# Performance work log

Measured on AMD Instinct MI355X. Metric: run time of the kernel, lower is better.

## Reference

```python
import jax, jax.numpy as jnp
import numpy as np

EMBED_DIM = 1024
NUM_HEADS = 16
HEAD_DIM = EMBED_DIM // NUM_HEADS
B, SQ, SKV = 2, 2048, 2048


def setup_inputs() -> dict:
    key = jax.random.key(0)
    ks = jax.random.split(key, 12)
    s = 1.0 / np.sqrt(EMBED_DIM)
    inp = {
        "query": jax.random.normal(ks[0], (B, SQ, EMBED_DIM), jnp.float32),
        "key": jax.random.normal(ks[1], (B, SKV, EMBED_DIM), jnp.float32),
        "value": jax.random.normal(ks[2], (B, SKV, EMBED_DIM), jnp.float32),
        "Wq": jax.random.normal(ks[3], (EMBED_DIM, EMBED_DIM), jnp.float32) * s,
        "bq": jnp.zeros((EMBED_DIM,), jnp.float32),
        "Wk": jax.random.normal(ks[4], (EMBED_DIM, EMBED_DIM), jnp.float32) * s,
        "bk": jnp.zeros((EMBED_DIM,), jnp.float32),
        "Wv": jax.random.normal(ks[5], (EMBED_DIM, EMBED_DIM), jnp.float32) * s,
        "bv": jnp.zeros((EMBED_DIM,), jnp.float32),
        "Wo": jax.random.normal(ks[6], (EMBED_DIM, EMBED_DIM), jnp.float32) * s,
        "bo": jnp.zeros((EMBED_DIM,), jnp.float32),
        "ln_gamma": jnp.ones((EMBED_DIM,), jnp.float32),
        "ln_beta": jnp.zeros((EMBED_DIM,), jnp.float32),
    }
    return inp


def reference(query, key, value, Wq, bq, Wk, bk, Wv, bv, Wo, bo, ln_gamma, ln_beta):
    b, sq, d = query.shape
    skv = key.shape[1]
    residual = query
    # projections -> [b, h, s, hd]
    Q = (query @ Wq + bq).reshape(b, sq, NUM_HEADS, HEAD_DIM).transpose(0, 2, 1, 3)
    K = (key @ Wk + bk).reshape(b, skv, NUM_HEADS, HEAD_DIM).transpose(0, 2, 1, 3)
    V = (value @ Wv + bv).reshape(b, skv, NUM_HEADS, HEAD_DIM).transpose(0, 2, 1, 3)
    scores = jnp.einsum("bhqd,bhkd->bhqk", Q, K) / jnp.sqrt(jnp.float32(HEAD_DIM)).astype(Q.dtype)
    attn = jax.nn.softmax(scores, axis=-1)  # dropout identity in eval
    attended = jnp.einsum("bhqk,bhkd->bhqd", attn, V)
    attended = attended.transpose(0, 2, 1, 3).reshape(b, sq, d)
    out = attended @ Wo + bo
    x = out + residual
    mu = jnp.mean(x, axis=-1, keepdims=True)
    var = jnp.var(x, axis=-1, keepdims=True)
    return (x - mu) / jnp.sqrt(var + 1e-5) * ln_gamma + ln_beta
```

## Files before the change

kernel.cpp:

```cpp
#include <hip/hip_runtime.h>

#define EMBED 1024
#define NHEAD 16
#define HDIM  64
#define BATCH 2
#define SEQ   2048
#define ROWS  (BATCH*SEQ)

typedef __bf16 bf16x8 __attribute__((ext_vector_type(8)));
typedef float  f32x4  __attribute__((ext_vector_type(4)));
typedef float  f32x16 __attribute__((ext_vector_type(16)));
typedef unsigned short u16x8 __attribute__((ext_vector_type(8)));
typedef unsigned short u16x4 __attribute__((ext_vector_type(4)));

__device__ __forceinline__ unsigned short f2bf(float f) {
    unsigned int u = __float_as_uint(f);
    u += 0x7FFFu + ((u >> 16) & 1u);
    return (unsigned short)(u >> 16);
}
__device__ __forceinline__ f32x4 zero4() { f32x4 z = {0.f, 0.f, 0.f, 0.f}; return z; }

__device__ __forceinline__ unsigned int cvtpk_bf16(float lo, float hi) {
    unsigned int r;
    asm("v_cvt_pk_bf16_f32 %0, %1, %2" : "=v"(r) : "v"(lo), "v"(hi));
    return r;
}
__device__ __forceinline__ void pl32swap(unsigned int &a, unsigned int &b) {
    asm("v_permlane32_swap_b32 %0, %1" : "+v"(a), "+v"(b));
}
__device__ __forceinline__ float exp2_hw(float x) {
    float r;
    asm("v_exp_f32 %0, %1" : "=v"(r) : "v"(x));
    return r;
}

__device__ __forceinline__ void gl_lds16(const unsigned short* g, unsigned short* l) {
    __builtin_amdgcn_global_load_lds(
        (const __attribute__((address_space(1))) void*)g,
        (__attribute__((address_space(3))) void*)l, 16, 0, 0);
}

__global__ __launch_bounds__(256) void cvt3_kernel(const float* __restrict__ q,
                                                   const float* __restrict__ k,
                                                   const float* __restrict__ v,
                                                   unsigned short* __restrict__ qo,
                                                   unsigned short* __restrict__ ko,
                                                   unsigned short* __restrict__ vo) {
    const float* in; unsigned short* out;
    if (blockIdx.y == 0)      { in = q; out = qo; }
    else if (blockIdx.y == 1) { in = k; out = ko; }
    else                      { in = v; out = vo; }
    int i = (blockIdx.x * 256 + threadIdx.x) * 4;
    float4 vv = *(const float4*)(in + i);
    u16x4 o = {f2bf(vv.x), f2bf(vv.y), f2bf(vv.z), f2bf(vv.w)};
    *(u16x4*)(out + i) = o;
}

__global__ __launch_bounds__(256) void transpose4_kernel(const float* __restrict__ w0,
                                                         const float* __restrict__ w1,
                                                         const float* __restrict__ w2,
                                                         const float* __restrict__ w3,
                                                         unsigned short* __restrict__ o0,
                                                         unsigned short* __restrict__ o1,
                                                         unsigned short* __restrict__ o2,
                                                         unsigned short* __restrict__ o3) {
    const float* in; unsigned short* out;
    if (blockIdx.z == 0)      { in = w0; out = o0; }
    else if (blockIdx.z == 1) { in = w1; out = o1; }
    else if (blockIdx.z == 2) { in = w2; out = o2; }
    else                      { in = w3; out = o3; }
    __shared__ float tile[32][33];
    int tx = threadIdx.x, ty = threadIdx.y;
    int x = blockIdx.x * 32 + tx;
    int y0 = blockIdx.y * 32 + ty;
#pragma unroll
    for (int r = 0; r < 4; ++r)
        tile[ty + 8 * r][tx] = in[(size_t)(y0 + 8 * r) * EMBED + x];
    __syncthreads();
    int ox = blockIdx.y * 32 + tx;
    int oy = blockIdx.x * 32 + ty;
#pragma unroll
    for (int r = 0; r < 4; ++r)
        out[(size_t)(oy + 8 * r) * EMBED + ox] = f2bf(tile[tx][ty + 8 * r]);
}

__global__ __launch_bounds__(256, 2) void gemm_qkv_kernel(
    const unsigned short* __restrict__ qb, const unsigned short* __restrict__ kb,
    const unsigned short* __restrict__ vb,
    const unsigned short* __restrict__ Wqt, const unsigned short* __restrict__ Wkt,
    const unsigned short* __restrict__ Wvt,
    const float* __restrict__ bq, const float* __restrict__ bk, const float* __restrict__ bv,
    unsigned short* __restrict__ Qp, unsigned short* __restrict__ Kp,
    unsigned short* __restrict__ Vtb) {
    __shared__ unsigned short smem[24576];
    const unsigned short *A, *Bt; const float* bias; unsigned short* outp; int mode; float osc;
    if (blockIdx.z == 0)      { A = qb; Bt = Wqt; bias = bq; outp = Qp;  mode = 0; osc = 0.18033688f; }
    else if (blockIdx.z == 1) { A = kb; Bt = Wkt; bias = bk; outp = Kp;  mode = 0; osc = 1.0f; }
    else                      { A = vb; Bt = Wvt; bias = bv; outp = Vtb; mode = 1; osc = 1.0f; }

    const int t = threadIdx.x;
    const int m0 = blockIdx.x * 128, n0 = blockIdx.y * 128;
    const int wave = t >> 6, lane = t & 63;
    const int wr = wave >> 1, wc = wave & 1;
    const int lm = lane & 15, lq = lane >> 4;
    const int sr = t >> 2;
    const int csrc = (t & 3) ^ ((sr >> 1) & 3);
    const int pa = lq ^ ((lm >> 1) & 3);

    const unsigned short* gA = A + (size_t)(m0 + sr) * EMBED + csrc * 8;
    const unsigned short* gB = Bt + (size_t)(n0 + sr) * EMBED + csrc * 8;

    f32x4 acc[4][4];
#pragma unroll
    for (int i = 0; i < 4; ++i)
#pragma unroll
        for (int j = 0; j < 4; ++j) acc[i][j] = zero4();

#define QKV_STAGE(SOFF)                                                      \
    gl_lds16(gA,              smem + (SOFF) + wave * 512);                   \
    gl_lds16(gA + 64 * EMBED, smem + (SOFF) + 2048 + wave * 512);            \
    gl_lds16(gB,              smem + 12288 + (SOFF) + wave * 512);           \
    gl_lds16(gB + 64 * EMBED, smem + 12288 + (SOFF) + 2048 + wave * 512);    \
    gA += 32; gB += 32;

#define QKV_COMP(COFF)                                                                 \
    {                                                                                  \
        bf16x8 af[4], bfr[4];                                                          \
        _Pragma("unroll")                                                              \
        for (int i = 0; i < 4; ++i)                                                    \
            af[i] = *(const bf16x8*)&smem[(COFF) + (wr * 64 + i * 16 + lm) * 32 + pa * 8]; \
        _Pragma("unroll")                                                              \
        for (int j = 0; j < 4; ++j)                                                    \
            bfr[j] = *(const bf16x8*)&smem[12288 + (COFF) + (wc * 64 + j * 16 + lm) * 32 + pa * 8]; \
        _Pragma("unroll")                                                              \
        for (int i = 0; i < 4; ++i)                                                    \
            _Pragma("unroll")                                                          \
            for (int j = 0; j < 4; ++j)                                                \
                acc[i][j] = __builtin_amdgcn_mfma_f32_16x16x32_bf16(af[i], bfr[j], acc[i][j], 0, 0, 0); \
    }

    QKV_STAGE(0)
    QKV_STAGE(4096)

    for (int g = 0; g < 10; ++g) {
        asm volatile("s_waitcnt vmcnt(4)" ::: "memory");
        __builtin_amdgcn_s_barrier();
        QKV_STAGE(8192)
        QKV_COMP(0)
        asm volatile("s_waitcnt vmcnt(4)" ::: "memory");
        __builtin_amdgcn_s_barrier();
        QKV_STAGE(0)
        QKV_COMP(4096)
        asm volatile("s_waitcnt vmcnt(4)" ::: "memory");
        __builtin_amdgcn_s_barrier();
        QKV_STAGE(4096)
        QKV_COMP(8192)
    }
    asm volatile("s_waitcnt vmcnt(4)" ::: "memory");
    __builtin_amdgcn_s_barrier();
    QKV_COMP(0)
    asm volatile("s_waitcnt vmcnt(0)" ::: "memory");
    __builtin_amdgcn_s_barrier();
    QKV_COMP(4096)

    const int row = t >> 2, seg = t & 3;
    if (mode == 0) {
#pragma unroll
        for (int p = 0; p < 2; ++p) {
            __syncthreads();
            if (wr == p) {
#pragma unroll
                for (int i = 0; i < 4; ++i)
#pragma unroll
                    for (int j = 0; j < 4; ++j) {
                        float bn = bias[n0 + wc * 64 + j * 16 + lm];
                        int nl = wc * 64 + j * 16 + lm;
#pragma unroll
                        for (int r = 0; r < 4; ++r)
                            smem[(i * 16 + lq * 4 + r) * 136 + nl] =
                                f2bf((acc[i][j][r] + bn) * osc);
                    }
            }
            __syncthreads();
            int m = m0 + p * 64 + row;
            int b = m >> 11, sI = m & 2047;
            int ncol = n0 + seg * 32;
            int h = ncol >> 6, hd0 = ncol & 63;
            unsigned short* dst = outp + (((size_t)((b * NHEAD + h) * SEQ + sI)) << 6) + hd0;
            const unsigned short* src = smem + row * 136 + seg * 32;
            *(u16x8*)(dst)      = *(const u16x8*)(src);
            *(u16x8*)(dst + 8)  = *(const u16x8*)(src + 8);
            *(u16x8*)(dst + 16) = *(const u16x8*)(src + 16);
            *(u16x8*)(dst + 24) = *(const u16x8*)(src + 24);
        }
    } else {
#pragma unroll
        for (int p = 0; p < 2; ++p) {
            __syncthreads();
            if (wc == p) {
#pragma unroll
                for (int i = 0; i < 4; ++i)
#pragma unroll
                    for (int j = 0; j < 4; ++j) {
                        float bn = bias[n0 + p * 64 + j * 16 + lm];
                        u16x4 pw = {f2bf(acc[i][j][0] + bn), f2bf(acc[i][j][1] + bn),
                                    f2bf(acc[i][j][2] + bn), f2bf(acc[i][j][3] + bn)};
                        *(u16x4*)&smem[(j * 16 + lm) * 136 + wr * 64 + i * 16 + lq * 4] = pw;
                    }
            }
            __syncthreads();
            int n = n0 + p * 64 + row;
            int h = n >> 6, hd = n & 63;
            int b = m0 >> 11;
            int s0 = (m0 & 2047) + seg * 32;
            unsigned short* dst = outp + ((size_t)((b * NHEAD + h) * HDIM + hd)) * SEQ + s0;
            const unsigned short* src = smem + row * 136 + seg * 32;
            *(u16x8*)(dst)      = *(const u16x8*)(src);
            *(u16x8*)(dst + 8)  = *(const u16x8*)(src + 8);
            *(u16x8*)(dst + 16) = *(const u16x8*)(src + 16);
            *(u16x8*)(dst + 24) = *(const u16x8*)(src + 24);
        }
    }
#undef QKV_STAGE
#undef QKV_COMP
}

__global__ __launch_bounds__(256, 2) void gemm_o_kernel(
    const unsigned short* __restrict__ att, const unsigned short* __restrict__ Wot,
    const float* __restrict__ bo, float* __restrict__ xbuf,
    const float* __restrict__ residual) {
    __shared__ unsigned short smem[18432];
    const int t = threadIdx.x;
    const int m0 = blockIdx.x * 64, n0 = blockIdx.y * 128;
    const int wave = t >> 6, lane = t & 63;
    const int lm = lane & 15, lq = lane >> 4;
    const int sr = t >> 2;
    const int csrc = (t & 3) ^ ((sr >> 1) & 3);
    const int pa = lq ^ ((lm >> 1) & 3);

    const unsigned short* gA = att + (size_t)(m0 + sr) * EMBED + csrc * 8;
    const unsigned short* gB = Wot + (size_t)(n0 + sr) * EMBED + csrc * 8;

    f32x4 acc[4][2];
#pragma unroll
    for (int i = 0; i < 4; ++i)
#pragma unroll
        for (int j = 0; j < 2; ++j) acc[i][j] = zero4();

#define O_STAGE(SA, SB)                                                  \
    gl_lds16(gA,              smem + (SA) + wave * 512);                 \
    gl_lds16(gB,              smem + 6144 + (SB) + wave * 512);          \
    gl_lds16(gB + 64 * EMBED, smem + 6144 + (SB) + 2048 + wave * 512);   \
    gA += 32; gB += 32;

#define O_COMP(SA, SB)                                                                \
    {                                                                                 \
        bf16x8 af[4], bfr[2];                                                         \
        _Pragma("unroll")                                                             \
        for (int i = 0; i < 4; ++i)                                                   \
            af[i] = *(const bf16x8*)&smem[(SA) + (i * 16 + lm) * 32 + pa * 8];        \
        _Pragma("unroll")                                                             \
        for (int j = 0; j < 2; ++j)                                                   \
            bfr[j] = *(const bf16x8*)&smem[6144 + (SB) + (wave * 32 + j * 16 + lm) * 32 + pa * 8]; \
        _Pragma("unroll")                                                             \
        for (int i = 0; i < 4; ++i)                                                   \
            _Pragma("unroll")                                                         \
            for (int j = 0; j < 2; ++j)                                               \
                acc[i][j] = __builtin_amdgcn_mfma_f32_16x16x32_bf16(af[i], bfr[j], acc[i][j], 0, 0, 0); \
    }

    O_STAGE(0, 0)
    O_STAGE(2048, 4096)

    for (int g = 0; g < 10; ++g) {
        asm volatile("s_waitcnt vmcnt(3)" ::: "memory");
        __builtin_amdgcn_s_barrier();
        O_STAGE(4096, 8192)
        O_COMP(0, 0)
        asm volatile("s_waitcnt vmcnt(3)" ::: "memory");
        __builtin_amdgcn_s_barrier();
        O_STAGE(0, 0)
        O_COMP(2048, 4096)
        asm volatile("s_waitcnt vmcnt(3)" ::: "memory");
        __builtin_amdgcn_s_barrier();
        O_STAGE(2048, 4096)
        O_COMP(4096, 8192)
    }
    asm volatile("s_waitcnt vmcnt(3)" ::: "memory");
    __builtin_amdgcn_s_barrier();
    O_COMP(0, 0)
    asm volatile("s_waitcnt vmcnt(0)" ::: "memory");
    __builtin_amdgcn_s_barrier();
    O_COMP(2048, 4096)

#pragma unroll
    for (int i = 0; i < 4; ++i)
#pragma unroll
        for (int j = 0; j < 2; ++j) {
            int n = n0 + wave * 32 + j * 16 + lm;
            float bn = bo[n];
#pragma unroll
            for (int r = 0; r < 4; ++r) {
                int m = m0 + i * 16 + lq * 4 + r;
                size_t idx = (size_t)m * EMBED + n;
                xbuf[idx] = acc[i][j][r] + bn + residual[idx];
            }
        }
#undef O_STAGE
#undef O_COMP
}

__global__ __launch_bounds__(256, 2) void attn_kernel(const unsigned short* __restrict__ Qp,
                                                      const unsigned short* __restrict__ Kp,
                                                      const unsigned short* __restrict__ Vt,
                                                      unsigned short* __restrict__ att) {
    __shared__ unsigned short Ks[16384];
    __shared__ unsigned short Vs[16384];
    const int t = threadIdx.x;
    const int bh = blockIdx.x;
    const int b = bh >> 4, h = bh & 15;
    const int q0 = blockIdx.y * 128;
    const unsigned short* Qh = Qp + (size_t)bh * SEQ * HDIM;
    const unsigned short* Kh = Kp + (size_t)bh * SEQ * HDIM;
    const unsigned short* Vh = Vt + (size_t)bh * HDIM * SEQ;
    const int wave = t >> 6, lane = t & 63;
    const int ln31 = lane & 31, half = lane >> 5;

    bf16x8 qf[4];
    {
        const unsigned short* qptr = Qh + (size_t)(q0 + wave * 32 + ln31) * HDIM + half * 8;
#pragma unroll
        for (int s = 0; s < 4; ++s) qf[s] = *(const bf16x8*)(qptr + s * 16);
    }

    const int q8a = t, q8b = 256 + t;
    const int fa = q8a >> 6, fb = q8b >> 6;
    const int ma = q8a & 31, mb = q8b & 31;
    const int ha = (q8a >> 5) & 1, hb = (q8b >> 5) & 1;
    const unsigned short* gK0 = Kh + (size_t)((fa >> 2) * 32 + ma) * HDIM + (fa & 3) * 16 + ha * 8;
    const unsigned short* gK1 = Kh + (size_t)((fb >> 2) * 32 + mb) * HDIM + (fb & 3) * 16 + hb * 8;
    const unsigned short* gV0 = Vh + (size_t)((fa >> 2) * 32 + ma) * SEQ + (fa & 3) * 16 + ha * 8;
    const unsigned short* gV1 = Vh + (size_t)((fb >> 2) * 32 + mb) * SEQ + (fb & 3) * 16 + hb * 8;

    gl_lds16(gK0,              Ks + wave * 512);
    gl_lds16(gK1,              Ks + 2048 + wave * 512);
    gl_lds16(gK0 + 64 * HDIM,  Ks + 4096 + wave * 512);
    gl_lds16(gK1 + 64 * HDIM,  Ks + 4096 + 2048 + wave * 512);
    gl_lds16(gV0,              Vs + wave * 512);
    gl_lds16(gV1,              Vs + 2048 + wave * 512);
    gl_lds16(gV0 + 64,         Vs + 4096 + wave * 512);
    gl_lds16(gV1 + 64,         Vs + 4096 + 2048 + wave * 512);
    gK0 += 128 * HDIM; gK1 += 128 * HDIM; gV0 += 128; gV1 += 128;
    gl_lds16(gK0,              Ks + 8192 + wave * 512);
    gl_lds16(gK1,              Ks + 8192 + 2048 + wave * 512);
    gl_lds16(gK0 + 64 * HDIM,  Ks + 8192 + 4096 + wave * 512);
    gl_lds16(gK1 + 64 * HDIM,  Ks + 8192 + 4096 + 2048 + wave * 512);
    gl_lds16(gV0,              Vs + 8192 + wave * 512);
    gl_lds16(gV1,              Vs + 8192 + 2048 + wave * 512);
    gl_lds16(gV0 + 64,         Vs + 8192 + 4096 + wave * 512);
    gl_lds16(gV1 + 64,         Vs + 8192 + 4096 + 2048 + wave * 512);
    gK0 += 128 * HDIM; gK1 += 128 * HDIM; gV0 += 128; gV1 += 128;

    f32x16 OFFS;
#pragma unroll
    for (int r = 0; r < 16; ++r) OFFS[r] = -17.312340f;

    f32x16 Oa[2][2];
#pragma unroll
    for (int mo = 0; mo < 2; ++mo)
#pragma unroll
        for (int pr = 0; pr < 2; ++pr)
#pragma unroll
            for (int r = 0; r < 16; ++r) Oa[mo][pr][r] = 0.f;
    float rpA = 0.f, rpB = 0.f, rpC = 0.f, rpD = 0.f;

    for (int kt2 = 0; kt2 < 16; ++kt2) {
        if (kt2 < 15) { asm volatile("s_waitcnt vmcnt(8)" ::: "memory"); }
        else          { asm volatile("s_waitcnt vmcnt(0)" ::: "memory"); }
        __builtin_amdgcn_s_barrier();
        const int cbo = (kt2 & 1) * 8192;

        f32x16 S[2][2];
        __builtin_amdgcn_s_setprio(1);
#pragma unroll
        for (int tl = 0; tl < 2; ++tl)
#pragma unroll
            for (int mt = 0; mt < 2; ++mt) {
                {
                    bf16x8 af = *(const bf16x8*)&Ks[cbo + tl * 4096 + (mt * 4 + 0) * 512 + half * 256 + ln31 * 8];
                    S[tl][mt] = __builtin_amdgcn_mfma_f32_32x32x16_bf16(af, qf[0], OFFS, 0, 0, 0);
                }
#pragma unroll
                for (int s = 1; s < 4; ++s) {
                    bf16x8 af = *(const bf16x8*)&Ks[cbo + tl * 4096 + (mt * 4 + s) * 512 + half * 256 + ln31 * 8];
                    S[tl][mt] = __builtin_amdgcn_mfma_f32_32x32x16_bf16(af, qf[s], S[tl][mt], 0, 0, 0);
                }
            }
        __builtin_amdgcn_s_setprio(0);

#pragma unroll
        for (int tl = 0; tl < 2; ++tl) {
#pragma unroll
            for (int mt = 0; mt < 2; ++mt)
#pragma unroll
                for (int rg = 0; rg < 4; ++rg) {
                    float p0 = exp2_hw(S[tl][mt][rg * 4 + 0]);
                    float p1 = exp2_hw(S[tl][mt][rg * 4 + 1]);
                    float p2 = exp2_hw(S[tl][mt][rg * 4 + 2]);
                    float p3 = exp2_hw(S[tl][mt][rg * 4 + 3]);
                    S[tl][mt][rg * 4 + 0] = p0; rpA += p0;
                    S[tl][mt][rg * 4 + 1] = p1; rpB += p1;
                    S[tl][mt][rg * 4 + 2] = p2; rpC += p2;
                    S[tl][mt][rg * 4 + 3] = p3; rpD += p3;
                }

            __builtin_amdgcn_s_setprio(1);
#pragma unroll
            for (int mt = 0; mt < 2; ++mt)
#pragma unroll
                for (int p = 0; p < 2; ++p) {
                    unsigned int a0 = cvtpk_bf16(S[tl][mt][8 * p + 0], S[tl][mt][8 * p + 1]);
                    unsigned int a1 = cvtpk_bf16(S[tl][mt][8 * p + 2], S[tl][mt][8 * p + 3]);
                    unsigned int b0 = cvtpk_bf16(S[tl][mt][8 * p + 4], S[tl][mt][8 * p + 5]);
                    unsigned int b1 = cvtpk_bf16(S[tl][mt][8 * p + 6], S[tl][mt][8 * p + 7]);
                    pl32swap(a0, b0);
                    pl32swap(a1, b1);
                    union { unsigned int u[4]; bf16x8 v; } bp;
                    bp.u[0] = a0; bp.u[1] = a1; bp.u[2] = b0; bp.u[3] = b1;
                    const int sp = mt * 2 + p;
#pragma unroll
                    for (int mo = 0; mo < 2; ++mo) {
                        bf16x8 av = *(const bf16x8*)&Vs[cbo + tl * 4096 + (mo * 4 + sp) * 512 + half * 256 + ln31 * 8];
                        Oa[mo][p] = __builtin_amdgcn_mfma_f32_32x32x16_bf16(av, bp.v, Oa[mo][p], 0, 0, 0);
                    }
                }
            __builtin_amdgcn_s_setprio(0);
        }

        if (kt2 < 14) {
            __builtin_amdgcn_s_barrier();
            gl_lds16(gK0,              Ks + cbo + wave * 512);
            gl_lds16(gK1,              Ks + cbo + 2048 + wave * 512);
            gl_lds16(gK0 + 64 * HDIM,  Ks + cbo + 4096 + wave * 512);
            gl_lds16(gK1 + 64 * HDIM,  Ks + cbo + 4096 + 2048 + wave * 512);
            gl_lds16(gV0,              Vs + cbo + wave * 512);
            gl_lds16(gV1,              Vs + cbo + 2048 + wave * 512);
            gl_lds16(gV0 + 64,         Vs + cbo + 4096 + wave * 512);
            gl_lds16(gV1 + 64,         Vs + cbo + 4096 + 2048 + wave * 512);
            gK0 += 128 * HDIM; gK1 += 128 * HDIM; gV0 += 128; gV1 += 128;
        }
    }

    float l_loc = (rpA + rpB) + (rpC + rpD);
    unsigned int la = __float_as_uint(l_loc), lb = __float_as_uint(l_loc);
    pl32swap(la, lb);
    float inv = 1.f / (__uint_as_float(la) + __uint_as_float(lb));

    int q = q0 + wave * 32 + ln31;
    unsigned short* orow = att + (size_t)(b * SEQ + q) * EMBED + h * HDIM;
#pragma unroll
    for (int mo = 0; mo < 2; ++mo)
#pragma unroll
        for (int rg = 0; rg < 4; ++rg) {
            u16x4 ow = {f2bf((Oa[mo][0][rg * 4 + 0] + Oa[mo][1][rg * 4 + 0]) * inv),
                        f2bf((Oa[mo][0][rg * 4 + 1] + Oa[mo][1][rg * 4 + 1]) * inv),
                        f2bf((Oa[mo][0][rg * 4 + 2] + Oa[mo][1][rg * 4 + 2]) * inv),
                        f2bf((Oa[mo][0][rg * 4 + 3] + Oa[mo][1][rg * 4 + 3]) * inv)};
            *(u16x4*)&orow[mo * 32 + rg * 8 + half * 4] = ow;
        }
}

__global__ __launch_bounds__(256) void ln_kernel(const float* __restrict__ x,
                                                 const float* __restrict__ gamma,
                                                 const float* __restrict__ beta,
                                                 float* __restrict__ out) {
    __shared__ float red[8];
    const int row = blockIdx.x, t = threadIdx.x;
    float4 v = *(const float4*)(x + (size_t)row * EMBED + t * 4);
    float s = v.x + v.y + v.z + v.w;
    float ss = v.x * v.x + v.y * v.y + v.z * v.z + v.w * v.w;
#pragma unroll
    for (int o = 1; o < 64; o <<= 1) {
        s += __shfl_xor(s, o);
        ss += __shfl_xor(ss, o);
    }
    int wave = t >> 6, lane = t & 63;
    if (lane == 0) { red[wave] = s; red[4 + wave] = ss; }
    __syncthreads();
    s = red[0] + red[1] + red[2] + red[3];
    ss = red[4] + red[5] + red[6] + red[7];
    float mu = s * (1.f / EMBED);
    float var = ss * (1.f / EMBED) - mu * mu;
    float rstd = rsqrtf(var + 1e-5f);
    float4 g = *(const float4*)(gamma + t * 4);
    float4 bb = *(const float4*)(beta + t * 4);
    float4 o;
    o.x = (v.x - mu) * rstd * g.x + bb.x;
    o.y = (v.y - mu) * rstd * g.y + bb.y;
    o.z = (v.z - mu) * rstd * g.z + bb.z;
    o.w = (v.w - mu) * rstd * g.w + bb.w;
    *(float4*)(out + (size_t)row * EMBED + t * 4) = o;
}

extern "C" void kernel_launch(void* const* d_in, const int* in_sizes, int n_in,
                              void* d_out, int out_size, void* d_ws, size_t ws_size,
                              hipStream_t stream) {
    const float* query = (const float*)d_in[0];
    const float* key_  = (const float*)d_in[1];
    const float* value = (const float*)d_in[2];
    const float* Wq = (const float*)d_in[3];
    const float* bq = (const float*)d_in[4];
    const float* Wk = (const float*)d_in[5];
    const float* bk = (const float*)d_in[6];
    const float* Wv = (const float*)d_in[7];
    const float* bv = (const float*)d_in[8];
    const float* Wo = (const float*)d_in[9];
    const float* bo = (const float*)d_in[10];
    const float* gamma = (const float*)d_in[11];
    const float* beta  = (const float*)d_in[12];

    char* ws = (char*)d_ws;
    const size_t MB = 1024 * 1024;
    unsigned short* qb  = (unsigned short*)(ws + 0);
    unsigned short* kb  = (unsigned short*)(ws + 8 * MB);
    unsigned short* vb  = (unsigned short*)(ws + 16 * MB);
    unsigned short* Wqt = (unsigned short*)(ws + 24 * MB);
    unsigned short* Wkt = (unsigned short*)(ws + 26 * MB);
    unsigned short* Wvt = (unsigned short*)(ws + 28 * MB);
    unsigned short* Wot = (unsigned short*)(ws + 30 * MB);
    unsigned short* Qp  = (unsigned short*)(ws + 32 * MB);
    unsigned short* Kp  = (unsigned short*)(ws + 40 * MB);
    unsigned short* Vtb = (unsigned short*)(ws + 48 * MB);
    unsigned short* att = (unsigned short*)(ws + 0);
    float*          xbuf = (float*)(ws + 8 * MB);

    cvt3_kernel<<<dim3(4096, 3), 256, 0, stream>>>(query, key_, value, qb, kb, vb);
    transpose4_kernel<<<dim3(32, 32, 4), dim3(32, 8), 0, stream>>>(Wq, Wk, Wv, Wo, Wqt, Wkt, Wvt, Wot);

    gemm_qkv_kernel<<<dim3(32, 8, 3), 256, 0, stream>>>(qb, kb, vb, Wqt, Wkt, Wvt,
                                                        bq, bk, bv, Qp, Kp, Vtb);

    attn_kernel<<<dim3(32, 16), 256, 0, stream>>>(Qp, Kp, Vtb, att);

    gemm_o_kernel<<<dim3(64, 8), 256, 0, stream>>>(att, Wot, bo, xbuf, query);
    ln_kernel<<<ROWS, 256, 0, stream>>>(xbuf, gamma, beta, (float*)d_out);
}
```

Measured before the change: 227.4 us.

## Split attention KV tiles across two wave groups with LDS output reduction

The attention kernel moves to 512 threads per block: two groups of four waves share the same 128 query rows, and each group handles half of every 128-key tile, so S/P register state per wave is halved. Partial outputs and row sums from group 1 are passed to group 0 through LDS at the end, where they are added and normalised. The grid is flattened to 1D with the query-tile index in the low bits, so blocks for the same head run close together. This aims for more waves in flight and better latency hiding, but it adds an LDS reduction step, one more barrier, and more waves contending at each tile barrier.

```diff
diff --git a/kernel.cpp b/kernel.cpp
--- a/kernel.cpp
+++ b/kernel.cpp
@@ -310,164 +310,156 @@
 #undef O_COMP
 }
 
-__global__ __launch_bounds__(256, 2) void attn_kernel(const unsigned short* __restrict__ Qp,
+__global__ __launch_bounds__(512, 4) void attn_kernel(const unsigned short* __restrict__ Qp,
                                                       const unsigned short* __restrict__ Kp,
                                                       const unsigned short* __restrict__ Vt,
                                                       unsigned short* __restrict__ att) {
-    __shared__ unsigned short Ks[16384];
-    __shared__ unsigned short Vs[16384];
+    __shared__ unsigned short KV[32768];
+    unsigned short* Ks = KV;
+    unsigned short* Vs = KV + 16384;
     const int t = threadIdx.x;
-    const int bh = blockIdx.x;
+    const int bx = blockIdx.x;
+    const int bh = bx >> 4;
     const int b = bh >> 4, h = bh & 15;
-    const int q0 = blockIdx.y * 128;
+    const int q0 = (bx & 15) * 128;
     const unsigned short* Qh = Qp + (size_t)bh * SEQ * HDIM;
     const unsigned short* Kh = Kp + (size_t)bh * SEQ * HDIM;
     const unsigned short* Vh = Vt + (size_t)bh * HDIM * SEQ;
     const int wave = t >> 6, lane = t & 63;
-    const int ln31 = lane & 31, half = lane >> 5;
+    const int g = wave >> 2, ws = wave & 3;
+    const int ln31 = lane & 31, halfl = lane >> 5;
 
     bf16x8 qf[4];
     {
-        const unsigned short* qptr = Qh + (size_t)(q0 + wave * 32 + ln31) * HDIM + half * 8;
+        const unsigned short* qptr = Qh + (size_t)(q0 + ws * 32 + ln31) * HDIM + halfl * 8;
 #pragma unroll
         for (int s = 0; s < 4; ++s) qf[s] = *(const bf16x8*)(qptr + s * 16);
     }
 
-    const int q8a = t, q8b = 256 + t;
-    const int fa = q8a >> 6, fb = q8b >> 6;
-    const int ma = q8a & 31, mb = q8b & 31;
-    const int ha = (q8a >> 5) & 1, hb = (q8b >> 5) & 1;
-    const unsigned short* gK0 = Kh + (size_t)((fa >> 2) * 32 + ma) * HDIM + (fa & 3) * 16 + ha * 8;
-    const unsigned short* gK1 = Kh + (size_t)((fb >> 2) * 32 + mb) * HDIM + (fb & 3) * 16 + hb * 8;
-    const unsigned short* gV0 = Vh + (size_t)((fa >> 2) * 32 + ma) * SEQ + (fa & 3) * 16 + ha * 8;
-    const unsigned short* gV1 = Vh + (size_t)((fb >> 2) * 32 + mb) * SEQ + (fb & 3) * 16 + hb * 8;
-
-    gl_lds16(gK0,              Ks + wave * 512);
-    gl_lds16(gK1,              Ks + 2048 + wave * 512);
-    gl_lds16(gK0 + 64 * HDIM,  Ks + 4096 + wave * 512);
-    gl_lds16(gK1 + 64 * HDIM,  Ks + 4096 + 2048 + wave * 512);
-    gl_lds16(gV0,              Vs + wave * 512);
-    gl_lds16(gV1,              Vs + 2048 + wave * 512);
-    gl_lds16(gV0 + 64,         Vs + 4096 + wave * 512);
-    gl_lds16(gV1 + 64,         Vs + 4096 + 2048 + wave * 512);
-    gK0 += 128 * HDIM; gK1 += 128 * HDIM; gV0 += 128; gV1 += 128;
-    gl_lds16(gK0,              Ks + 8192 + wave * 512);
-    gl_lds16(gK1,              Ks + 8192 + 2048 + wave * 512);
-    gl_lds16(gK0 + 64 * HDIM,  Ks + 8192 + 4096 + wave * 512);
-    gl_lds16(gK1 + 64 * HDIM,  Ks + 8192 + 4096 + 2048 + wave * 512);
-    gl_lds16(gV0,              Vs + 8192 + wave * 512);
-    gl_lds16(gV1,              Vs + 8192 + 2048 + wave * 512);
-    gl_lds16(gV0 + 64,         Vs + 8192 + 4096 + wave * 512);
-    gl_lds16(gV1 + 64,         Vs + 8192 + 4096 + 2048 + wave * 512);
-    gK0 += 128 * HDIM; gK1 += 128 * HDIM; gV0 += 128; gV1 += 128;
+    const int f0 = t >> 6, m0_ = t & 31, hh0 = (t >> 5) & 1;
+    const unsigned short* gK0 = Kh + (size_t)((f0 >> 2) * 32 + m0_) * HDIM + (f0 & 3) * 16 + hh0 * 8;
+    const unsigned short* gV0 = Vh + (size_t)((f0 >> 2) * 32 + m0_) * SEQ + (f0 & 3) * 16 + hh0 * 8;
+
+#define ATTN_STAGE(NBO)                                                   \
+    gl_lds16(gK0,             Ks + (NBO) + wave * 512);                   \
+    gl_lds16(gK0 + 64 * HDIM, Ks + (NBO) + 4096 + wave * 512);            \
+    gl_lds16(gV0,             Vs + (NBO) + wave * 512);                   \
+    gl_lds16(gV0 + 64,        Vs + (NBO) + 4096 + wave * 512);            \
+    gK0 += 128 * HDIM; gV0 += 128;
+
+    ATTN_STAGE(0)
+    ATTN_STAGE(8192)
 
     f32x16 OFFS;
 #pragma unroll
     for (int r = 0; r < 16; ++r) OFFS[r] = -17.312340f;
 
-    f32x16 Oa[2][2];
+    f32x16 Oa[2];
 #pragma unroll
     for (int mo = 0; mo < 2; ++mo)
 #pragma unroll
-        for (int pr = 0; pr < 2; ++pr)
-#pragma unroll
-            for (int r = 0; r < 16; ++r) Oa[mo][pr][r] = 0.f;
+        for (int r = 0; r < 16; ++r) Oa[mo][r] = 0.f;
     float rpA = 0.f, rpB = 0.f, rpC = 0.f, rpD = 0.f;
 
-    for (int kt2 = 0; kt2 < 16; ++kt2) {
-        if (kt2 < 15) { asm volatile("s_waitcnt vmcnt(8)" ::: "memory"); }
-        else          { asm volatile("s_waitcnt vmcnt(0)" ::: "memory"); }
-        __builtin_amdgcn_s_barrier();
-        const int cbo = (kt2 & 1) * 8192;
-
-        f32x16 S[2][2];
-        __builtin_amdgcn_s_setprio(1);
-#pragma unroll
-        for (int tl = 0; tl < 2; ++tl)
-#pragma unroll
-            for (int mt = 0; mt < 2; ++mt) {
-                {
-                    bf16x8 af = *(const bf16x8*)&Ks[cbo + tl * 4096 + (mt * 4 + 0) * 512 + half * 256 + ln31 * 8];
-                    S[tl][mt] = __builtin_amdgcn_mfma_f32_32x32x16_bf16(af, qf[0], OFFS, 0, 0, 0);
+    for (int kt = 0; kt < 16; ++kt) {
+        if (kt < 15) { asm volatile("s_waitcnt vmcnt(4)" ::: "memory"); }
+        else         { asm volatile("s_waitcnt vmcnt(0)" ::: "memory"); }
+        __builtin_amdgcn_s_barrier();
+        const int cbo = (kt & 1) * 8192 + g * 4096;
+
+#pragma unroll
+        for (int mt = 0; mt < 2; ++mt) {
+            f32x16 S;
+            __builtin_amdgcn_s_setprio(1);
+            {
+                bf16x8 af = *(const bf16x8*)&Ks[cbo + (mt * 4 + 0) * 512 + halfl * 256 + ln31 * 8];
+                S = __builtin_amdgcn_mfma_f32_32x32x16_bf16(af, qf[0], OFFS, 0, 0, 0);
+            }
+#pragma unroll
+            for (int s = 1; s < 4; ++s) {
+                bf16x8 af = *(const bf16x8*)&Ks[cbo + (mt * 4 + s) * 512 + halfl * 256 + ln31 * 8];
+                S = __builtin_amdgcn_mfma_f32_32x32x16_bf16(af, qf[s], S, 0, 0, 0);
+            }
+            __builtin_amdgcn_s_setprio(0);
+
+#pragma unroll
+            for (int rg = 0; rg < 4; ++rg) {
+                float p0 = exp2_hw(S[rg * 4 + 0]);
+                float p1 = exp2_hw(S[rg * 4 + 1]);
+                float p2 = exp2_hw(S[rg * 4 + 2]);
+                float p3 = exp2_hw(S[rg * 4 + 3]);
+                S[rg * 4 + 0] = p0; rpA += p0;
+                S[rg * 4 + 1] = p1; rpB += p1;
+                S[rg * 4 + 2] = p2; rpC += p2;
+                S[rg * 4 + 3] = p3; rpD += p3;
+            }
+
+            __builtin_amdgcn_s_setprio(1);
+#pragma unroll
+            for (int p = 0; p < 2; ++p) {
+                unsigned int a0 = cvtpk_bf16(S[8 * p + 0], S[8 * p + 1]);
+                unsigned int a1 = cvtpk_bf16(S[8 * p + 2], S[8 * p + 3]);
+                unsigned int b0 = cvtpk_bf16(S[8 * p + 4], S[8 * p + 5]);
+                unsigned int b1 = cvtpk_bf16(S[8 * p + 6], S[8 * p + 7]);
+                pl32swap(a0, b0);
+                pl32swap(a1, b1);
+                union { unsigned int u[4]; bf16x8 v; } bp;
+                bp.u[0] = a0; bp.u[1] = a1; bp.u[2] = b0; bp.u[3] = b1;
+                const int sp = mt * 2 + p;
+#pragma unroll
+                for (int mo = 0; mo < 2; ++mo) {
+                    bf16x8 av = *(const bf16x8*)&Vs[cbo + (mo * 4 + sp) * 512 + halfl * 256 + ln31 * 8];
+                    Oa[mo] = __builtin_amdgcn_mfma_f32_32x32x16_bf16(av, bp.v, Oa[mo], 0, 0, 0);
                 }
-#pragma unroll
-                for (int s = 1; s < 4; ++s) {
-                    bf16x8 af = *(const bf16x8*)&Ks[cbo + tl * 4096 + (mt * 4 + s) * 512 + half * 256 + ln31 * 8];
-                    S[tl][mt] = __builtin_amdgcn_mfma_f32_32x32x16_bf16(af, qf[s], S[tl][mt], 0, 0, 0);
-                }
-            }
-        __builtin_amdgcn_s_setprio(0);
-
-#pragma unroll
-        for (int tl = 0; tl < 2; ++tl) {
-#pragma unroll
-            for (int mt = 0; mt < 2; ++mt)
-#pragma unroll
-                for (int rg = 0; rg < 4; ++rg) {
-                    float p0 = exp2_hw(S[tl][mt][rg * 4 + 0]);
-                    float p1 = exp2_hw(S[tl][mt][rg * 4 + 1]);
-                    float p2 = exp2_hw(S[tl][mt][rg * 4 + 2]);
-                    float p3 = exp2_hw(S[tl][mt][rg * 4 + 3]);
-                    S[tl][mt][rg * 4 + 0] = p0; rpA += p0;
-                    S[tl][mt][rg * 4 + 1] = p1; rpB += p1;
-                    S[tl][mt][rg * 4 + 2] = p2; rpC += p2;
-                    S[tl][mt][rg * 4 + 3] = p3; rpD += p3;
-                }
-
-            __builtin_amdgcn_s_setprio(1);
-#pragma unroll
-            for (int mt = 0; mt < 2; ++mt)
-#pragma unroll
-                for (int p = 0; p < 2; ++p) {
-                    unsigned int a0 = cvtpk_bf16(S[tl][mt][8 * p + 0], S[tl][mt][8 * p + 1]);
-                    unsigned int a1 = cvtpk_bf16(S[tl][mt][8 * p + 2], S[tl][mt][8 * p + 3]);
-                    unsigned int b0 = cvtpk_bf16(S[tl][mt][8 * p + 4], S[tl][mt][8 * p + 5]);
-                    unsigned int b1 = cvtpk_bf16(S[tl][mt][8 * p + 6], S[tl][mt][8 * p + 7]);
-                    pl32swap(a0, b0);
-                    pl32swap(a1, b1);
-                    union { unsigned int u[4]; bf16x8 v; } bp;
-                    bp.u[0] = a0; bp.u[1] = a1; bp.u[2] = b0; bp.u[3] = b1;
-                    const int sp = mt * 2 + p;
-#pragma unroll
-                    for (int mo = 0; mo < 2; ++mo) {
-                        bf16x8 av = *(const bf16x8*)&Vs[cbo + tl * 4096 + (mo * 4 + sp) * 512 + half * 256 + ln31 * 8];
-                        Oa[mo][p] = __builtin_amdgcn_mfma_f32_32x32x16_bf16(av, bp.v, Oa[mo][p], 0, 0, 0);
-                    }
-                }
+            }
             __builtin_amdgcn_s_setprio(0);
         }
 
-        if (kt2 < 14) {
+        if (kt < 14) {
             __builtin_amdgcn_s_barrier();
-            gl_lds16(gK0,              Ks + cbo + wave * 512);
-            gl_lds16(gK1,              Ks + cbo + 2048 + wave * 512);
-            gl_lds16(gK0 + 64 * HDIM,  Ks + cbo + 4096 + wave * 512);
-            gl_lds16(gK1 + 64 * HDIM,  Ks + cbo + 4096 + 2048 + wave * 512);
-            gl_lds16(gV0,              Vs + cbo + wave * 512);
-            gl_lds16(gV1,              Vs + cbo + 2048 + wave * 512);
-            gl_lds16(gV0 + 64,         Vs + cbo + 4096 + wave * 512);
-            gl_lds16(gV1 + 64,         Vs + cbo + 4096 + 2048 + wave * 512);
-            gK0 += 128 * HDIM; gK1 += 128 * HDIM; gV0 += 128; gV1 += 128;
+            const int nbo = (kt & 1) * 8192;
+            ATTN_STAGE(nbo)
         }
     }
-
-    float l_loc = (rpA + rpB) + (rpC + rpD);
-    unsigned int la = __float_as_uint(l_loc), lb = __float_as_uint(l_loc);
+#undef ATTN_STAGE
+
+    float lsum = (rpA + rpB) + (rpC + rpD);
+    unsigned int la = __float_as_uint(lsum), lb = __float_as_uint(lsum);
     pl32swap(la, lb);
-    float inv = 1.f / (__uint_as_float(la) + __uint_as_float(lb));
-
-    int q = q0 + wave * 32 + ln31;
-    unsigned short* orow = att + (size_t)(b * SEQ + q) * EMBED + h * HDIM;
-#pragma unroll
-    for (int mo = 0; mo < 2; ++mo)
-#pragma unroll
-        for (int rg = 0; rg < 4; ++rg) {
-            u16x4 ow = {f2bf((Oa[mo][0][rg * 4 + 0] + Oa[mo][1][rg * 4 + 0]) * inv),
-                        f2bf((Oa[mo][0][rg * 4 + 1] + Oa[mo][1][rg * 4 + 1]) * inv),
-                        f2bf((Oa[mo][0][rg * 4 + 2] + Oa[mo][1][rg * 4 + 2]) * inv),
-                        f2bf((Oa[mo][0][rg * 4 + 3] + Oa[mo][1][rg * 4 + 3]) * inv)};
-            *(u16x4*)&orow[mo * 32 + rg * 8 + half * 4] = ow;
-        }
+    float ltot = __uint_as_float(la) + __uint_as_float(lb);
+
+    __syncthreads();
+    float* shO = (float*)KV;
+    float* shL = (float*)KV + 128 * 68;
+    const int qr = ws * 32 + ln31;
+    if (g == 1) {
+#pragma unroll
+        for (int mo = 0; mo < 2; ++mo)
+#pragma unroll
+            for (int rg = 0; rg < 4; ++rg) {
+                float4 v;
+                v.x = Oa[mo][rg * 4 + 0]; v.y = Oa[mo][rg * 4 + 1];
+                v.z = Oa[mo][rg * 4 + 2]; v.w = Oa[mo][rg * 4 + 3];
+                *(float4*)&shO[qr * 68 + mo * 32 + rg * 8 + halfl * 4] = v;
+            }
+        shL[qr] = ltot;
+    }
+    __syncthreads();
+    if (g == 0) {
+        float inv = 1.f / (ltot + shL[qr]);
+        unsigned short* orow = att + (size_t)(b * SEQ + q0 + qr) * EMBED + h * HDIM;
+#pragma unroll
+        for (int mo = 0; mo < 2; ++mo)
+#pragma unroll
+            for (int rg = 0; rg < 4; ++rg) {
+                float4 v = *(const float4*)&shO[qr * 68 + mo * 32 + rg * 8 + halfl * 4];
+                u16x4 ow = {f2bf((Oa[mo][rg * 4 + 0] + v.x) * inv),
+                            f2bf((Oa[mo][rg * 4 + 1] + v.y) * inv),
+                            f2bf((Oa[mo][rg * 4 + 2] + v.z) * inv),
+                            f2bf((Oa[mo][rg * 4 + 3] + v.w) * inv)};
+                *(u16x4*)&orow[mo * 32 + rg * 8 + halfl * 4] = ow;
+            }
+    }
 }
 
 __global__ __launch_bounds__(256) void ln_kernel(const float* __restrict__ x,
@@ -540,7 +532,7 @@
     gemm_qkv_kernel<<<dim3(32, 8, 3), 256, 0, stream>>>(qb, kb, vb, Wqt, Wkt, Wvt,
                                                         bq, bk, bv, Qp, Kp, Vtb);
 
-    attn_kernel<<<dim3(32, 16), 256, 0, stream>>>(Qp, Kp, Vtb, att);
+    attn_kernel<<<dim3(512), 512, 0, stream>>>(Qp, Kp, Vtb, att);
 
     gemm_o_kernel<<<dim3(64, 8), 256, 0, stream>>>(att, Wot, bo, xbuf, query);
     ln_kernel<<<ROWS, 256, 0, stream>>>(xbuf, gamma, beta, (float*)d_out);
```

Result: no change. 228.1 us (+0.3%).
